# Performance work log

Measured on AMD Instinct MI355X. Metric: run time of the kernel, lower is better.

Reference implementation:

```python
import jax, jax.numpy as jnp
import numpy as np
from jax.scipy.linalg import solve_triangular

EPS = 2e-5

def setup_inputs() -> dict:
    key = jax.random.key(0)
    k1, k2 = jax.random.split(key)
    B, N, H, W = 8, 256, 128, 128
    cont_feat = jax.random.normal(k1, (B, N, H, W), dtype=jnp.float32)
    styl_feat = jax.random.normal(k2, (B, N, H, W), dtype=jnp.float32)
    return {"cont_feat": cont_feat, "styl_feat": styl_feat}

def _cov(x):
    # x: [B, N, L], already centered. Returns [B, N, N]
    L = x.shape[-1]
    c = jnp.einsum('bnl,bml->bnm', x, x) / (L - 1)
    # eps jitter for Cholesky stability (original retries with eps on failure)
    return c + EPS * jnp.eye(x.shape[1], dtype=x.dtype)

def reference(cont_feat, styl_feat):
    B, N, cH, cW = cont_feat.shape
    xc = cont_feat.reshape(B, N, -1)
    xs = styl_feat.reshape(B, N, -1)

    # whitening of content
    c_mean = jnp.mean(xc, axis=-1, keepdims=True)
    xc_c = xc - c_mean
    Lc = jnp.linalg.cholesky(_cov(xc_c))           # [B, N, N] lower
    whiten_c = solve_triangular(Lc, xc_c, lower=True)  # == inv(Lc) @ xc_c

    # coloring with style statistics
    s_mean = jnp.mean(xs, axis=-1, keepdims=True)
    xs_c = xs - s_mean
    Ls = jnp.linalg.cholesky(_cov(xs_c))
    color = jnp.einsum('bnm,bml->bnl', Ls, whiten_c) + s_mean

    return color.reshape(B, N, cH, cW)
```

## Files before the change

### kernel.cpp

```cpp
#include <hip/hip_runtime.h>


#define BATCH 8
#define NF    256
#define LSP   16384
#define EPS_J 2e-5f

typedef float f32x4  __attribute__((ext_vector_type(4)));
typedef short bf16x8 __attribute__((ext_vector_type(8)));
typedef short short4v __attribute__((ext_vector_type(4)));

__device__ __forceinline__ short f2bf(float f) {
    unsigned u = __float_as_uint(f);
    u = (u + 0x7FFFu + ((u >> 16) & 1u)) >> 16;
    return (short)u;
}
__device__ __forceinline__ float bf2f(short s) {
    return __uint_as_float(((unsigned)(unsigned short)s) << 16);
}

__device__ __forceinline__ void tri_map(int w, int& ti, int& tj) {
    ti = (w >= 6) ? 3 : ((w >= 3) ? 2 : ((w >= 1) ? 1 : 0));
    tj = w - ti * (ti + 1) / 2;
}

__global__ __launch_bounds__(1024, 4) void k_cov(const float* __restrict__ cont,
                                                 const float* __restrict__ styl,
                                                 float* __restrict__ gram,
                                                 float* __restrict__ rowsum,
                                                 float* __restrict__ part,
                                                 int use_part) {
    const int kc = blockIdx.x;
    const int m  = blockIdx.y;
    const float* __restrict__ src = (m < BATCH)
        ? cont + (size_t)m * NF * LSP
        : styl + (size_t)(m - BATCH) * NF * LSP;

    __shared__ short lds[256][72];

    const int t    = threadIdx.x;
    const int lane = t & 63;
    const int w    = t >> 6;
    int ti = 0, tj = 0;
    tri_map(w < 10 ? w : 0, ti, tj);
    const int wi = ti * 64;
    const int wj = tj * 64;
    const int fr = t >> 4;
    const int fc = (t & 15) * 4;

    f32x4 acc[4][4];
    #pragma unroll
    for (int i = 0; i < 4; ++i)
        #pragma unroll
        for (int j = 0; j < 4; ++j) { f32x4 z = {0.f,0.f,0.f,0.f}; acc[i][j] = z; }

    float rs[4] = {0.f, 0.f, 0.f, 0.f};

    const size_t kbase = (size_t)kc * 1024;
    float4 pre[4];
    #pragma unroll
    for (int j = 0; j < 4; ++j)
        pre[j] = *(const float4*)(src + (size_t)(fr + j * 64) * LSP + kbase + fc);

    for (int step = 0; step < 16; ++step) {
        __syncthreads();
        #pragma unroll
        for (int j = 0; j < 4; ++j) {
            float4 v = pre[j];
            rs[j] += v.x + v.y + v.z + v.w;
            short4v b4 = { f2bf(v.x), f2bf(v.y), f2bf(v.z), f2bf(v.w) };
            *(short4v*)&lds[fr + j * 64][fc] = b4;
        }
        __syncthreads();
        if (step < 15) {
            const size_t k0n = kbase + (size_t)(step + 1) * 64;
            #pragma unroll
            for (int j = 0; j < 4; ++j)
                pre[j] = *(const float4*)(src + (size_t)(fr + j * 64) * LSP + k0n + fc);
        }
        if (w < 10) {
            #pragma unroll
            for (int ks = 0; ks < 2; ++ks) {
                const int kk   = ks * 32 + (lane >> 4) * 8;
                const int rsel = lane & 15;
                bf16x8 af[4], bfv[4];
                #pragma unroll
                for (int mi = 0; mi < 4; ++mi)
                    af[mi] = *(const bf16x8*)&lds[wi + mi * 16 + rsel][kk];
                #pragma unroll
                for (int nj = 0; nj < 4; ++nj)
                    bfv[nj] = *(const bf16x8*)&lds[wj + nj * 16 + rsel][kk];
                #pragma unroll
                for (int mi = 0; mi < 4; ++mi)
                    #pragma unroll
                    for (int nj = 0; nj < 4; ++nj)
                        acc[mi][nj] = __builtin_amdgcn_mfma_f32_16x16x32_bf16(
                            af[mi], bfv[nj], acc[mi][nj], 0, 0, 0);
            }
        }
    }

    float* rsm = rowsum + m * NF;
    #pragma unroll
    for (int j = 0; j < 4; ++j) {
        float v = rs[j];
        v += __shfl_xor(v, 1);
        v += __shfl_xor(v, 2);
        v += __shfl_xor(v, 4);
        v += __shfl_xor(v, 8);
        if ((lane & 15) == 0) atomicAdd(rsm + fr + j * 64, v);
    }

    if (w >= 10) return;

    const int rowb = (lane >> 4) * 4;
    const int colb = lane & 15;
    if (use_part) {
        float* __restrict__ pt = part + (((size_t)m * 16 + kc) * 10 + w) * 4096;
        #pragma unroll
        for (int mi = 0; mi < 4; ++mi)
            #pragma unroll
            for (int nj = 0; nj < 4; ++nj) {
                const int rl = mi * 16 + rowb;
                const int cl = nj * 16 + colb;
                #pragma unroll
                for (int r = 0; r < 4; ++r)
                    pt[(size_t)(rl + r) * 64 + cl] = acc[mi][nj][r];
            }
    } else {
        float* g = gram + (size_t)m * NF * NF;
        #pragma unroll
        for (int mi = 0; mi < 4; ++mi)
            #pragma unroll
            for (int nj = 0; nj < 4; ++nj) {
                const int row = wi + mi * 16 + rowb;
                const int col = wj + nj * 16 + colb;
                #pragma unroll
                for (int r = 0; r < 4; ++r)
                    atomicAdd(g + (size_t)(row + r) * NF + col, acc[mi][nj][r]);
            }
    }
}

__global__ __launch_bounds__(256) void k_reduce(const float* __restrict__ part,
                                                float* __restrict__ gram) {
    const int m  = blockIdx.x / 10;
    const int tt = blockIdx.x % 10;
    int ti, tj;
    tri_map(tt, ti, tj);
    const float* __restrict__ base = part + ((size_t)m * 16 * 10 + tt) * 4096;
    float* __restrict__ g = gram + (size_t)m * NF * NF;
    for (int e = threadIdx.x; e < 4096; e += 256) {
        float s = 0.f;
        #pragma unroll
        for (int sp = 0; sp < 16; ++sp)
            s += base[(size_t)sp * 10 * 4096 + e];
        g[(size_t)(ti * 64 + (e >> 6)) * NF + tj * 64 + (e & 63)] = s;
    }
}


__device__ __forceinline__ void load_split_frag(const float* Lt, int row, int jb,
                                                int lane, bf16x8& h, bf16x8& l) {
    const int koff = (lane >> 4) * 8;
    const int base = ((row * (row + 1)) >> 1) + jb + koff;
    #pragma unroll
    for (int u = 0; u < 8; ++u) {
        const float f = Lt[base + u];
        const short hh = f2bf(f);
        h[u] = hh;
        l[u] = f2bf(f - bf2f(hh));
    }
}

__device__ __forceinline__ void apply_tile(int tile, bf16x8 ph, bf16x8 pl,
                                           float* Lt, short (*Pb)[40],
                                           const short (*Whs)[40],
                                           const short (*Wls)[40],
                                           int jb, int R0, int lane) {
    const int r0   = (tile >> 1) * 16;
    const int c0   = (tile & 1) * 16;
    const int koff = (lane >> 4) * 8;
    bf16x8 wh = *(const bf16x8*)&Whs[c0 + (lane & 15)][koff];
    bf16x8 wl = *(const bf16x8*)&Wls[c0 + (lane & 15)][koff];
    f32x4 acc = {0.f, 0.f, 0.f, 0.f};
    acc = __builtin_amdgcn_mfma_f32_16x16x32_bf16(ph, wh, acc, 0, 0, 0);
    acc = __builtin_amdgcn_mfma_f32_16x16x32_bf16(pl, wh, acc, 0, 0, 0);
    acc = __builtin_amdgcn_mfma_f32_16x16x32_bf16(ph, wl, acc, 0, 0, 0);
    const int col  = c0 + (lane & 15);
    const int rowb = r0 + (lane >> 4) * 4;
    #pragma unroll
    for (int rg = 0; rg < 4; ++rg) {
        const int rr  = rowb + rg;
        const int row = R0 + rr;
        Lt[((row * (row + 1)) >> 1) + jb + col] = acc[rg];
        Pb[rr][col] = f2bf(acc[rg]);
    }
}

__global__ __launch_bounds__(1024, 4) void k_chol(float* __restrict__ Lg_all,
                                                  const float* __restrict__ rowsum,
                                                  float* __restrict__ LcT_all,
                                                  float* __restrict__ mean_all) {
    const int m = blockIdx.x;
    float* __restrict__ Lg  = Lg_all + (size_t)m * NF * NF;
    float* __restrict__ LcT = (m < BATCH) ? (LcT_all + (size_t)m * NF * NF) : nullptr;

    __shared__ float Lt[32896];
    __shared__ float Sm[NF];
    __shared__ float Db[32][36];
    __shared__ short Whs[32][40];
    __shared__ short Wls[32][40];
    __shared__ short Pb[224][40];

    const int t    = threadIdx.x;
    const int lane = t & 63;
    const int wv   = t >> 6;

    if (t < NF) {
        float s = rowsum[m * NF + t];
        Sm[t] = s;
        mean_all[m * NF + t] = s * (1.f / (float)LSP);
    }
    __syncthreads();

    const float invLn  = 1.f / (float)LSP;
    const float invLm1 = 1.f / (float)(LSP - 1);
    for (int idx = t; idx < NF * NF; idx += 1024) {
        const int r = idx >> 8, c = idx & 255;
        if (c <= r) {
            float v = (Lg[idx] - Sm[r] * Sm[c] * invLn) * invLm1;
            if (c == r) v += EPS_J;
            Lt[((r * (r + 1)) >> 1) + c] = v;
        }
    }
    __syncthreads();

    for (int jb = 0; jb < NF; jb += 32) {
        const int R0 = jb + 32;
        const int R  = NF - R0;
        const int nT = (R >> 4) * 2;

        bf16x8 ph0, pl0, ph1, pl1;
        int tw0 = -1, tw1 = -1;
        if (wv > 0) {
            const int tb = wv - 1;
            if (tb < nT) {
                tw0 = tb;
                load_split_frag(Lt, R0 + (tb >> 1) * 16 + (lane & 15), jb, lane, ph0, pl0);
            }
            if (tb + 15 < nT) {
                tw1 = tb + 15;
                load_split_frag(Lt, R0 + ((tb + 15) >> 1) * 16 + (lane & 15), jb, lane, ph1, pl1);
            }
        } else if (t < 32) {
            const int r = t;
            const int rbase = (((jb + r) * (jb + r + 1)) >> 1) + jb;
            float a[32];
            #pragma unroll
            for (int c = 0; c < 32; ++c)
                a[c] = (c <= r) ? Lt[rbase + c] : 0.f;
            #pragma unroll
            for (int j = 0; j < 32; ++j) {
                const float ajv = a[j];
                const float d   = __shfl(ajv, j);
                const float rd  = __builtin_amdgcn_rcpf(d);
                const float rs  = __builtin_amdgcn_rsqf(d);
                const float sc  = ajv * rd;
                #pragma unroll
                for (int c = j + 1; c < 32; ++c)
                    a[c] -= sc * __shfl(ajv, c);
                a[j] = ajv * rs;
            }
            #pragma unroll
            for (int c = 0; c < 32; ++c)
                if (c <= r) Lt[rbase + c] = a[c];
            #pragma unroll
            for (int c4 = 0; c4 < 8; ++c4) {
                f32x4 v = { a[c4 * 4], a[c4 * 4 + 1], a[c4 * 4 + 2], a[c4 * 4 + 3] };
                *(f32x4*)&Db[r][c4 * 4] = v;
            }

            if (R > 0) {
                const int k = r;
                float wcol[32];
                #pragma unroll
                for (int c = 0; c < 32; ++c) wcol[c] = 0.f;
                #pragma unroll
                for (int c = 0; c < 32; ++c) {
                    float s = (c == k) ? 1.f : 0.f;
                    const int ng = c >> 2;
                    #pragma unroll
                    for (int g = 0; g <= 7; ++g) {
                        if (g <= ng) {
                            f32x4 dv = *(const f32x4*)&Db[c][g * 4];
                            s -= dv[0] * wcol[g * 4]     + dv[1] * wcol[g * 4 + 1]
                               + dv[2] * wcol[g * 4 + 2] + dv[3] * wcol[g * 4 + 3];
                        }
                    }
                    wcol[c] = s * __builtin_amdgcn_rcpf(Db[c][c]);
                }
                #pragma unroll
                for (int c = 0; c < 32; ++c) {
                    const float wv_ = wcol[c];
                    const short hh = f2bf(wv_);
                    Whs[c][k] = hh;
                    Wls[c][k] = f2bf(wv_ - bf2f(hh));
                }
            }
        }
        __syncthreads();

        if (tw0 >= 0) apply_tile(tw0, ph0, pl0, Lt, Pb, Whs, Wls, jb, R0, lane);
        if (tw1 >= 0) apply_tile(tw1, ph1, pl1, Lt, Pb, Whs, Wls, jb, R0, lane);
        __syncthreads();

        if (R > 0) {
            const int nt  = R >> 4;
            const int ntt = nt * (nt + 1) / 2;
            for (int tt = wv; tt < ntt; tt += 16) {
                int tr = (int)((sqrtf(8.f * (float)tt + 1.f) - 1.f) * 0.5f);
                while ((tr + 1) * (tr + 2) / 2 <= tt) ++tr;
                while (tr * (tr + 1) / 2 > tt) --tr;
                const int tc = tt - tr * (tr + 1) / 2;
                const int r0 = tr * 16, c0 = tc * 16;
                bf16x8 af  = *(const bf16x8*)&Pb[r0 + (lane & 15)][(lane >> 4) * 8];
                bf16x8 bfv = *(const bf16x8*)&Pb[c0 + (lane & 15)][(lane >> 4) * 8];
                f32x4 accv = {0.f, 0.f, 0.f, 0.f};
                accv = __builtin_amdgcn_mfma_f32_16x16x32_bf16(af, bfv, accv, 0, 0, 0);
                const int col  = R0 + c0 + (lane & 15);
                const int rowb = R0 + r0 + (lane >> 4) * 4;
                if (tr != tc) {
                    #pragma unroll
                    for (int rg = 0; rg < 4; ++rg) {
                        const int row = rowb + rg;
                        Lt[((row * (row + 1)) >> 1) + col] -= accv[rg];
                    }
                } else {
                    #pragma unroll
                    for (int rg = 0; rg < 4; ++rg) {
                        const int row = rowb + rg;
                        if (col <= row)
                            Lt[((row * (row + 1)) >> 1) + col] -= accv[rg];
                    }
                }
            }
        }
        __syncthreads();
    }

    if (LcT) {
        for (int idx = t; idx < NF * NF; idx += 1024) {
            const int cc = idx >> 8, rr = idx & 255;
            if (rr >= cc) LcT[idx] = Lt[((rr * (rr + 1)) >> 1) + cc];
        }
    } else {
        for (int idx = t; idx < NF * NF; idx += 1024) {
            const int r = idx >> 8, c = idx & 255;
            if (c <= r) Lg[idx] = Lt[((r * (r + 1)) >> 1) + c];
        }
    }
}

__global__ __launch_bounds__(256) void k_solveT(const float* __restrict__ Lg_all,
                                                const float* __restrict__ LcT_all,
                                                const float* __restrict__ mean_all,
                                                short* __restrict__ Tbf,
                                                float* __restrict__ bias) {
    const int lane = threadIdx.x & 63;
    const int wv   = threadIdx.x >> 6;
    const int task = blockIdx.x * 4 + wv;
    const int b    = task >> 8;
    const int i    = task & 255;
    const float* __restrict__ Ls  = Lg_all + (size_t)(BATCH + b) * NF * NF + (size_t)i * NF;
    const float* __restrict__ LcT = LcT_all + (size_t)b * NF * NF;

    __shared__ float vbuf[4][NF];
    float* vb = vbuf[wv];
    for (int k = lane; k < NF; k += 64) vb[k] = 0.f;

    int j = i;
    for (; j >= 1; j -= 2) {
        const float* __restrict__ r0 = LcT + (size_t)j * NF;
        const float* __restrict__ r1 = r0 - NF;
        float s0 = 0.f, s1 = 0.f;
        for (int k = j + 1 + lane; k <= i; k += 64) {
            const float tk = vb[k];
            s0 += tk * r0[k];
            s1 += tk * r1[k];
        }
        #pragma unroll
        for (int mm = 32; mm >= 1; mm >>= 1) {
            s0 += __shfl_xor(s0, mm);
            s1 += __shfl_xor(s1, mm);
        }
        if (lane == 0) {
            const float tj  = (Ls[j] - s0) / r0[j];
            const float tjm = (Ls[j - 1] - s1 - tj * r1[j]) / r1[j - 1];
            vb[j]     = tj;
            vb[j - 1] = tjm;
        }
    }
    if (j == 0) {
        const float* __restrict__ r0 = LcT;
        float s0 = 0.f;
        for (int k = 1 + lane; k <= i; k += 64) s0 += vb[k] * r0[k];
        #pragma unroll
        for (int mm = 32; mm >= 1; mm >>= 1) s0 += __shfl_xor(s0, mm);
        if (lane == 0) vb[0] = (Ls[0] - s0) / r0[0];
    }

    const float* __restrict__ cm  = mean_all + b * NF;
    const float* __restrict__ smn = mean_all + (BATCH + b) * NF;
    float dot = 0.f;
    for (int k = lane; k < NF; k += 64) dot += vb[k] * cm[k];
    #pragma unroll
    for (int mm = 32; mm >= 1; mm >>= 1) dot += __shfl_xor(dot, mm);
    if (lane == 0) bias[b * NF + i] = smn[i] - dot;

    short* __restrict__ Tr = Tbf + (size_t)b * NF * NF + (size_t)i * NF;
    const int k4 = lane * 4;
    short4v o = { f2bf(vb[k4]), f2bf(vb[k4 + 1]), f2bf(vb[k4 + 2]), f2bf(vb[k4 + 3]) };
    *(short4v*)&Tr[k4] = o;
}

__global__ __launch_bounds__(256) void k_out(const float* __restrict__ cont,
                                             const short* __restrict__ Tbf,
                                             const float* __restrict__ bias,
                                             float* __restrict__ out) {
    const int b  = blockIdx.y;
    const int l0 = blockIdx.x * 64;
    const float* __restrict__ X  = cont + (size_t)b * NF * LSP;
    const short* __restrict__ Tb = Tbf + (size_t)b * NF * NF;
    float* __restrict__ O = out + (size_t)b * NF * LSP;

    __shared__ short a_s[256][72];
    __shared__ short b_s[64][72];
    __shared__ float bias_s[NF];

    const int t    = threadIdx.x;
    const int lane = t & 63;
    const int w    = t >> 6;

    bias_s[t] = bias[b * NF + t];

    f32x4 acc[4][4];
    #pragma unroll
    for (int i = 0; i < 4; ++i)
        #pragma unroll
        for (int j = 0; j < 4; ++j) { f32x4 z = {0.f,0.f,0.f,0.f}; acc[i][j] = z; }

    const int kb = (t >> 4) * 4;
    const int lb = (t & 15) * 4;
    const int fr = t >> 4;
    const int fc = (t & 15) * 4;

    float4 xr[4];
    #pragma unroll
    for (int r = 0; r < 4; ++r)
        xr[r] = *(const float4*)(X + (size_t)(kb + r) * LSP + l0 + lb);

    for (int step = 0; step < 4; ++step) {
        const int k0 = step * 64;
        __syncthreads();
        #pragma unroll
        for (int s2 = 0; s2 < 16; ++s2) {
            const int row = fr + s2 * 16;
            *(short4v*)&a_s[row][fc] = *(const short4v*)(Tb + (size_t)row * NF + k0 + fc);
        }
        {
            short4v c0v = { f2bf(xr[0].x), f2bf(xr[1].x), f2bf(xr[2].x), f2bf(xr[3].x) };
            short4v c1v = { f2bf(xr[0].y), f2bf(xr[1].y), f2bf(xr[2].y), f2bf(xr[3].y) };
            short4v c2v = { f2bf(xr[0].z), f2bf(xr[1].z), f2bf(xr[2].z), f2bf(xr[3].z) };
            short4v c3v = { f2bf(xr[0].w), f2bf(xr[1].w), f2bf(xr[2].w), f2bf(xr[3].w) };
            *(short4v*)&b_s[lb + 0][kb] = c0v;
            *(short4v*)&b_s[lb + 1][kb] = c1v;
            *(short4v*)&b_s[lb + 2][kb] = c2v;
            *(short4v*)&b_s[lb + 3][kb] = c3v;
        }
        __syncthreads();
        if (step < 3) {
            const int k0n = k0 + 64;
            #pragma unroll
            for (int r = 0; r < 4; ++r)
                xr[r] = *(const float4*)(X + (size_t)(k0n + kb + r) * LSP + l0 + lb);
        }
        #pragma unroll
        for (int ks = 0; ks < 2; ++ks) {
            const int kk   = ks * 32 + (lane >> 4) * 8;
            const int rsel = lane & 15;
            bf16x8 af[4], bfv[4];
            #pragma unroll
            for (int mi = 0; mi < 4; ++mi)
                af[mi] = *(const bf16x8*)&a_s[w * 64 + mi * 16 + rsel][kk];
            #pragma unroll
            for (int nj = 0; nj < 4; ++nj)
                bfv[nj] = *(const bf16x8*)&b_s[nj * 16 + rsel][kk];
            #pragma unroll
            for (int mi = 0; mi < 4; ++mi)
                #pragma unroll
                for (int nj = 0; nj < 4; ++nj)
                    acc[mi][nj] = __builtin_amdgcn_mfma_f32_16x16x32_bf16(
                        af[mi], bfv[nj], acc[mi][nj], 0, 0, 0);
        }
    }

    #pragma unroll
    for (int mi = 0; mi < 4; ++mi) {
        const int row = w * 64 + mi * 16 + (lane >> 4) * 4;
        #pragma unroll
        for (int nj = 0; nj < 4; ++nj) {
            const int col = l0 + nj * 16 + (lane & 15);
            #pragma unroll
            for (int r = 0; r < 4; ++r)
                O[(size_t)(row + r) * LSP + col] = acc[mi][nj][r] + bias_s[row + r];
        }
    }
}

extern "C" void kernel_launch(void* const* d_in, const int* in_sizes, int n_in,
                              void* d_out, int out_size, void* d_ws, size_t ws_size,
                              hipStream_t stream) {
    (void)in_sizes; (void)n_in; (void)out_size;
    const float* cont = (const float*)d_in[0];
    const float* styl = (const float*)d_in[1];
    float* out = (float*)d_out;

    float* ws       = (float*)d_ws;
    float* gram     = ws;
    float* rowsum   = gram + 16 * 65536;
    float* mean_all = rowsum + 4096;
    float* bias     = mean_all + 4096;
    float* LcT      = bias + 2048;
    short* Tbf      = (short*)(LcT + 8 * 65536);
    float* part     = (float*)(Tbf + 8 * 65536);

    const size_t need = ((size_t)((char*)(part + (size_t)16 * 16 * 10 * 4096)
                                  - (char*)ws));
    const int use_part = (ws_size >= need) ? 1 : 0;

    if (use_part) {
        hipMemsetAsync(rowsum, 0, (size_t)4096 * sizeof(float), stream);
    } else {
        hipMemsetAsync(gram, 0, (size_t)(16 * 65536 + 4096) * sizeof(float), stream);
    }

    k_cov   <<<dim3(16, 16), 1024, 0, stream>>>(cont, styl, gram, rowsum, part, use_part);
    if (use_part)
        k_reduce<<<160, 256, 0, stream>>>(part, gram);
    k_chol  <<<16,           1024, 0, stream>>>(gram, rowsum, LcT, mean_all);
    k_solveT<<<512,          256,  0, stream>>>(gram, LcT, mean_all, Tbf, bias);
    k_out   <<<dim3(256, 8), 256,  0, stream>>>(cont, Tbf, bias, out);
}
```

Measured before the change: 698.6 us.

## Pipeline blocked Cholesky: factor next panel during trailing update, precompute packed covariance

The blocked Cholesky loop is restructured so that wave 0 updates the next diagonal block first and factors it, building its triangular inverse, while the other waves finish the trailing SYRK update. This removes one barrier-separated serial phase per panel. The panel apply now runs per 16-row stripe instead of per tile. The reduce kernel now applies the mean correction, scaling and jitter and writes packed-triangular covariance, so k_chol only does a vectorized copy into LDS. Warp shuffles are replaced with readlane, and the Db staging buffer is dropped. The packed layout depends on use_part, so the fallback path keeps the old conversion.

```diff
diff --git a/kernel.cpp b/kernel.cpp
--- a/kernel.cpp
+++ b/kernel.cpp
@@ -17,6 +17,9 @@
 }
 __device__ __forceinline__ float bf2f(short s) {
     return __uint_as_float(((unsigned)(unsigned short)s) << 16);
+}
+__device__ __forceinline__ float rlane(float v, int l) {
+    return __int_as_float(__builtin_amdgcn_readlane(__float_as_int(v), l));
 }
 
 __device__ __forceinline__ void tri_map(int w, int& ti, int& tj) {
@@ -143,22 +146,35 @@
 }
 
 __global__ __launch_bounds__(256) void k_reduce(const float* __restrict__ part,
-                                                float* __restrict__ gram) {
+                                                const float* __restrict__ rowsum,
+                                                float* __restrict__ covP) {
     const int m  = blockIdx.x / 10;
     const int tt = blockIdx.x % 10;
     int ti, tj;
     tri_map(tt, ti, tj);
+    __shared__ float smr[64], smc[64];
+    const float* __restrict__ rsb = rowsum + m * NF;
+    if (threadIdx.x < 64)        smr[threadIdx.x]      = rsb[ti * 64 + threadIdx.x];
+    else if (threadIdx.x < 128)  smc[threadIdx.x - 64] = rsb[tj * 64 + threadIdx.x - 64];
+    __syncthreads();
+    const float invLn  = 1.f / (float)LSP;
+    const float invLm1 = 1.f / (float)(LSP - 1);
     const float* __restrict__ base = part + ((size_t)m * 16 * 10 + tt) * 4096;
-    float* __restrict__ g = gram + (size_t)m * NF * NF;
+    float* __restrict__ cp = covP + (size_t)m * NF * NF;
     for (int e = threadIdx.x; e < 4096; e += 256) {
-        float s = 0.f;
-        #pragma unroll
-        for (int sp = 0; sp < 16; ++sp)
-            s += base[(size_t)sp * 10 * 4096 + e];
-        g[(size_t)(ti * 64 + (e >> 6)) * NF + tj * 64 + (e & 63)] = s;
-    }
-}
-
+        const int rl = e >> 6, cl = e & 63;
+        const int r = ti * 64 + rl, c = tj * 64 + cl;
+        if (c <= r) {
+            float s = 0.f;
+            #pragma unroll
+            for (int sp = 0; sp < 16; ++sp)
+                s += base[(size_t)sp * 10 * 4096 + e];
+            float v = (s - smr[rl] * smc[cl] * invLn) * invLm1;
+            if (c == r) v += EPS_J;
+            cp[((r * (r + 1)) >> 1) + c] = v;
+        }
+    }
+}
 
 __device__ __forceinline__ void load_split_frag(const float* Lt, int row, int jb,
                                                 int lane, bf16x8& h, bf16x8& l) {
@@ -173,42 +189,114 @@
     }
 }
 
-__device__ __forceinline__ void apply_tile(int tile, bf16x8 ph, bf16x8 pl,
-                                           float* Lt, short (*Pb)[40],
-                                           const short (*Whs)[40],
-                                           const short (*Wls)[40],
-                                           int jb, int R0, int lane) {
-    const int r0   = (tile >> 1) * 16;
-    const int c0   = (tile & 1) * 16;
+__device__ __forceinline__ void apply_stripe(int s, float* Lt, short (*Pb)[40],
+                                             const short (*Whs)[40],
+                                             const short (*Wls)[40],
+                                             int jb, int R0, int lane) {
+    bf16x8 ph, pl;
+    load_split_frag(Lt, R0 + s * 16 + (lane & 15), jb, lane, ph, pl);
     const int koff = (lane >> 4) * 8;
-    bf16x8 wh = *(const bf16x8*)&Whs[c0 + (lane & 15)][koff];
-    bf16x8 wl = *(const bf16x8*)&Wls[c0 + (lane & 15)][koff];
-    f32x4 acc = {0.f, 0.f, 0.f, 0.f};
-    acc = __builtin_amdgcn_mfma_f32_16x16x32_bf16(ph, wh, acc, 0, 0, 0);
-    acc = __builtin_amdgcn_mfma_f32_16x16x32_bf16(pl, wh, acc, 0, 0, 0);
-    acc = __builtin_amdgcn_mfma_f32_16x16x32_bf16(ph, wl, acc, 0, 0, 0);
-    const int col  = c0 + (lane & 15);
-    const int rowb = r0 + (lane >> 4) * 4;
-    #pragma unroll
-    for (int rg = 0; rg < 4; ++rg) {
-        const int rr  = rowb + rg;
-        const int row = R0 + rr;
-        Lt[((row * (row + 1)) >> 1) + jb + col] = acc[rg];
-        Pb[rr][col] = f2bf(acc[rg]);
+    #pragma unroll
+    for (int half = 0; half < 2; ++half) {
+        const int c0 = half * 16;
+        bf16x8 wh = *(const bf16x8*)&Whs[c0 + (lane & 15)][koff];
+        bf16x8 wl = *(const bf16x8*)&Wls[c0 + (lane & 15)][koff];
+        f32x4 acc = {0.f, 0.f, 0.f, 0.f};
+        acc = __builtin_amdgcn_mfma_f32_16x16x32_bf16(ph, wh, acc, 0, 0, 0);
+        acc = __builtin_amdgcn_mfma_f32_16x16x32_bf16(pl, wh, acc, 0, 0, 0);
+        acc = __builtin_amdgcn_mfma_f32_16x16x32_bf16(ph, wl, acc, 0, 0, 0);
+        const int col  = c0 + (lane & 15);
+        const int rowb = s * 16 + (lane >> 4) * 4;
+        #pragma unroll
+        for (int rg = 0; rg < 4; ++rg) {
+            const int rr  = rowb + rg;
+            const int row = R0 + rr;
+            Lt[((row * (row + 1)) >> 1) + jb + col] = acc[rg];
+            Pb[rr][col] = f2bf(acc[rg]);
+        }
+    }
+}
+
+__device__ __forceinline__ void syrk_tile(int tt, float* Lt, const short (*Pb)[40],
+                                          int R0, int lane) {
+    int tr = (int)((sqrtf(8.f * (float)tt + 1.f) - 1.f) * 0.5f);
+    while ((tr + 1) * (tr + 2) / 2 <= tt) ++tr;
+    while (tr * (tr + 1) / 2 > tt) --tr;
+    const int tc = tt - tr * (tr + 1) / 2;
+    const int r0 = tr * 16, c0 = tc * 16;
+    bf16x8 af  = *(const bf16x8*)&Pb[r0 + (lane & 15)][(lane >> 4) * 8];
+    bf16x8 bfv = *(const bf16x8*)&Pb[c0 + (lane & 15)][(lane >> 4) * 8];
+    f32x4 accv = {0.f, 0.f, 0.f, 0.f};
+    accv = __builtin_amdgcn_mfma_f32_16x16x32_bf16(af, bfv, accv, 0, 0, 0);
+    const int col  = R0 + c0 + (lane & 15);
+    const int rowb = R0 + r0 + (lane >> 4) * 4;
+    if (tr != tc) {
+        #pragma unroll
+        for (int rg = 0; rg < 4; ++rg) {
+            const int row = rowb + rg;
+            Lt[((row * (row + 1)) >> 1) + col] -= accv[rg];
+        }
+    } else {
+        #pragma unroll
+        for (int rg = 0; rg < 4; ++rg) {
+            const int row = rowb + rg;
+            if (col <= row)
+                Lt[((row * (row + 1)) >> 1) + col] -= accv[rg];
+        }
+    }
+}
+
+__device__ __forceinline__ void factor_and_winv(int jb, bool doW, float* Lt,
+                                                short (*Whs)[40], short (*Wls)[40],
+                                                int r) {
+    const int rbase = (((jb + r) * (jb + r + 1)) >> 1) + jb;
+    float a[32];
+    #pragma unroll
+    for (int c = 0; c < 32; ++c)
+        a[c] = (c <= r) ? Lt[rbase + c] : 0.f;
+    #pragma unroll
+    for (int j = 0; j < 32; ++j) {
+        const float ajv = a[j];
+        const float d   = rlane(ajv, j);
+        const float rd  = __builtin_amdgcn_rcpf(d);
+        const float rs  = __builtin_amdgcn_rsqf(d);
+        const float sc  = ajv * rd;
+        #pragma unroll
+        for (int c = j + 1; c < 32; ++c)
+            a[c] -= sc * rlane(ajv, c);
+        a[j] = ajv * rs;
+    }
+    #pragma unroll
+    for (int c = 0; c < 32; ++c)
+        if (c <= r) Lt[rbase + c] = a[c];
+    if (doW) {
+        const int k = r;
+        float wcol[32];
+        #pragma unroll
+        for (int c = 0; c < 32; ++c) {
+            float s = (c == k) ? 1.f : 0.f;
+            #pragma unroll
+            for (int j = 0; j < c; ++j)
+                s -= rlane(a[j], c) * wcol[j];
+            wcol[c] = s * __builtin_amdgcn_rcpf(rlane(a[c], c));
+            const short hh = f2bf(wcol[c]);
+            Whs[c][k] = hh;
+            Wls[c][k] = f2bf(wcol[c] - bf2f(hh));
+        }
     }
 }
 
 __global__ __launch_bounds__(1024, 4) void k_chol(float* __restrict__ Lg_all,
                                                   const float* __restrict__ rowsum,
                                                   float* __restrict__ LcT_all,
-                                                  float* __restrict__ mean_all) {
+                                                  float* __restrict__ mean_all,
+                                                  int use_part) {
     const int m = blockIdx.x;
     float* __restrict__ Lg  = Lg_all + (size_t)m * NF * NF;
     float* __restrict__ LcT = (m < BATCH) ? (LcT_all + (size_t)m * NF * NF) : nullptr;
 
     __shared__ float Lt[32896];
     __shared__ float Sm[NF];
-    __shared__ float Db[32][36];
     __shared__ short Whs[32][40];
     __shared__ short Wls[32][40];
     __shared__ short Pb[224][40];
@@ -224,127 +312,44 @@
     }
     __syncthreads();
 
-    const float invLn  = 1.f / (float)LSP;
-    const float invLm1 = 1.f / (float)(LSP - 1);
-    for (int idx = t; idx < NF * NF; idx += 1024) {
-        const int r = idx >> 8, c = idx & 255;
-        if (c <= r) {
-            float v = (Lg[idx] - Sm[r] * Sm[c] * invLn) * invLm1;
-            if (c == r) v += EPS_J;
-            Lt[((r * (r + 1)) >> 1) + c] = v;
+    if (use_part) {
+        for (int i4 = t; i4 < 8224; i4 += 1024)
+            ((f32x4*)Lt)[i4] = ((const f32x4*)Lg)[i4];
+    } else {
+        const float invLn  = 1.f / (float)LSP;
+        const float invLm1 = 1.f / (float)(LSP - 1);
+        for (int idx = t; idx < NF * NF; idx += 1024) {
+            const int r = idx >> 8, c = idx & 255;
+            if (c <= r) {
+                float v = (Lg[idx] - Sm[r] * Sm[c] * invLn) * invLm1;
+                if (c == r) v += EPS_J;
+                Lt[((r * (r + 1)) >> 1) + c] = v;
+            }
         }
     }
     __syncthreads();
 
-    for (int jb = 0; jb < NF; jb += 32) {
+    if (t < 32) factor_and_winv(0, true, Lt, Whs, Wls, t);
+    __syncthreads();
+
+    for (int p = 0; p < 7; ++p) {
+        const int jb = p * 32;
         const int R0 = jb + 32;
         const int R  = NF - R0;
-        const int nT = (R >> 4) * 2;
-
-        bf16x8 ph0, pl0, ph1, pl1;
-        int tw0 = -1, tw1 = -1;
-        if (wv > 0) {
-            const int tb = wv - 1;
-            if (tb < nT) {
-                tw0 = tb;
-                load_split_frag(Lt, R0 + (tb >> 1) * 16 + (lane & 15), jb, lane, ph0, pl0);
-            }
-            if (tb + 15 < nT) {
-                tw1 = tb + 15;
-                load_split_frag(Lt, R0 + ((tb + 15) >> 1) * 16 + (lane & 15), jb, lane, ph1, pl1);
-            }
-        } else if (t < 32) {
-            const int r = t;
-            const int rbase = (((jb + r) * (jb + r + 1)) >> 1) + jb;
-            float a[32];
-            #pragma unroll
-            for (int c = 0; c < 32; ++c)
-                a[c] = (c <= r) ? Lt[rbase + c] : 0.f;
-            #pragma unroll
-            for (int j = 0; j < 32; ++j) {
-                const float ajv = a[j];
-                const float d   = __shfl(ajv, j);
-                const float rd  = __builtin_amdgcn_rcpf(d);
-                const float rs  = __builtin_amdgcn_rsqf(d);
-                const float sc  = ajv * rd;
-                #pragma unroll
-                for (int c = j + 1; c < 32; ++c)
-                    a[c] -= sc * __shfl(ajv, c);
-                a[j] = ajv * rs;
-            }
-            #pragma unroll
-            for (int c = 0; c < 32; ++c)
-                if (c <= r) Lt[rbase + c] = a[c];
-            #pragma unroll
-            for (int c4 = 0; c4 < 8; ++c4) {
-                f32x4 v = { a[c4 * 4], a[c4 * 4 + 1], a[c4 * 4 + 2], a[c4 * 4 + 3] };
-                *(f32x4*)&Db[r][c4 * 4] = v;
-            }
-
-            if (R > 0) {
-                const int k = r;
-                float wcol[32];
-                #pragma unroll
-                for (int c = 0; c < 32; ++c) wcol[c] = 0.f;
-                #pragma unroll
-                for (int c = 0; c < 32; ++c) {
-                    float s = (c == k) ? 1.f : 0.f;
-                    const int ng = c >> 2;
-                    #pragma unroll
-                    for (int g = 0; g <= 7; ++g) {
-                        if (g <= ng) {
-                            f32x4 dv = *(const f32x4*)&Db[c][g * 4];
-                            s -= dv[0] * wcol[g * 4]     + dv[1] * wcol[g * 4 + 1]
-                               + dv[2] * wcol[g * 4 + 2] + dv[3] * wcol[g * 4 + 3];
-                        }
-                    }
-                    wcol[c] = s * __builtin_amdgcn_rcpf(Db[c][c]);
-                }
-                #pragma unroll
-                for (int c = 0; c < 32; ++c) {
-                    const float wv_ = wcol[c];
-                    const short hh = f2bf(wv_);
-                    Whs[c][k] = hh;
-                    Wls[c][k] = f2bf(wv_ - bf2f(hh));
-                }
-            }
-        }
+        const int nS = R >> 4;
+
+        if (wv < nS) apply_stripe(wv, Lt, Pb, Whs, Wls, jb, R0, lane);
         __syncthreads();
 
-        if (tw0 >= 0) apply_tile(tw0, ph0, pl0, Lt, Pb, Whs, Wls, jb, R0, lane);
-        if (tw1 >= 0) apply_tile(tw1, ph1, pl1, Lt, Pb, Whs, Wls, jb, R0, lane);
-        __syncthreads();
-
-        if (R > 0) {
-            const int nt  = R >> 4;
-            const int ntt = nt * (nt + 1) / 2;
-            for (int tt = wv; tt < ntt; tt += 16) {
-                int tr = (int)((sqrtf(8.f * (float)tt + 1.f) - 1.f) * 0.5f);
-                while ((tr + 1) * (tr + 2) / 2 <= tt) ++tr;
-                while (tr * (tr + 1) / 2 > tt) --tr;
-                const int tc = tt - tr * (tr + 1) / 2;
-                const int r0 = tr * 16, c0 = tc * 16;
-                bf16x8 af  = *(const bf16x8*)&Pb[r0 + (lane & 15)][(lane >> 4) * 8];
-                bf16x8 bfv = *(const bf16x8*)&Pb[c0 + (lane & 15)][(lane >> 4) * 8];
-                f32x4 accv = {0.f, 0.f, 0.f, 0.f};
-                accv = __builtin_amdgcn_mfma_f32_16x16x32_bf16(af, bfv, accv, 0, 0, 0);
-                const int col  = R0 + c0 + (lane & 15);
-                const int rowb = R0 + r0 + (lane >> 4) * 4;
-                if (tr != tc) {
-                    #pragma unroll
-                    for (int rg = 0; rg < 4; ++rg) {
-                        const int row = rowb + rg;
-                        Lt[((row * (row + 1)) >> 1) + col] -= accv[rg];
-                    }
-                } else {
-                    #pragma unroll
-                    for (int rg = 0; rg < 4; ++rg) {
-                        const int row = rowb + rg;
-                        if (col <= row)
-                            Lt[((row * (row + 1)) >> 1) + col] -= accv[rg];
-                    }
-                }
-            }
+        const int ntt = nS * (nS + 1) / 2;
+        if (wv == 0) {
+            syrk_tile(0, Lt, Pb, R0, lane);
+            syrk_tile(1, Lt, Pb, R0, lane);
+            syrk_tile(2, Lt, Pb, R0, lane);
+            if (t < 32) factor_and_winv(R0, (R - 32) > 0, Lt, Whs, Wls, t);
+        } else {
+            for (int tt = 2 + wv; tt < ntt; tt += 15)
+                syrk_tile(tt, Lt, Pb, R0, lane);
         }
         __syncthreads();
     }
@@ -547,8 +552,8 @@
 
     k_cov   <<<dim3(16, 16), 1024, 0, stream>>>(cont, styl, gram, rowsum, part, use_part);
     if (use_part)
-        k_reduce<<<160, 256, 0, stream>>>(part, gram);
-    k_chol  <<<16,           1024, 0, stream>>>(gram, rowsum, LcT, mean_all);
+        k_reduce<<<160, 256, 0, stream>>>(part, rowsum, gram);
+    k_chol  <<<16,           1024, 0, stream>>>(gram, rowsum, LcT, mean_all, use_part);
     k_solveT<<<512,          256,  0, stream>>>(gram, LcT, mean_all, Tbf, bias);
     k_out   <<<dim3(256, 8), 256,  0, stream>>>(cont, Tbf, bias, out);
 }
```

Result: faster. 622.8 us (-10.9%).
